# Optimization experiments

Measured on AMD Instinct MI355X. Metric: run time of the kernel, lower is better.

The kernel has to match this reference:

```python
import jax, jax.numpy as jnp
import numpy as np

MESSAGE_PASSES = 3  # constants.message_passes
F_NODE = 64   # hidden_node_features
F_EDGE = 16   # n_edge_features
M_MSG = 64    # message_size
OUT_DIM = 128
B, N = 8, 256
EDGE_DENSITY = 0.1


def setup_inputs() -> dict:
    key = jax.random.key(0)
    ks = jax.random.split(key, 12)
    nodes = jax.random.normal(ks[0], (B, N, F_NODE), dtype=jnp.float32)
    # sparse positive edge features: rand * bernoulli connectivity (avg degree ~ N*density)
    raw = jax.random.uniform(ks[1], (B, N, N, F_EDGE), dtype=jnp.float32)
    conn = (jax.random.uniform(ks[2], (B, N, N)) < EDGE_DENSITY).astype(jnp.float32)
    edges = raw * conn[..., None]
    s = 0.05
    return {
        "nodes": nodes,
        "edges": edges,
        # message MLP: cat(neighbour, edge) -> message_size
        "W_msg": jax.random.normal(ks[3], (F_NODE + F_EDGE, M_MSG), dtype=jnp.float32) * s,
        "b_msg": jnp.zeros((M_MSG,), dtype=jnp.float32),
        # GRU cell (input=message_size, hidden=F_NODE), gates [r|z|n]
        "W_i": jax.random.normal(ks[4], (M_MSG, 3 * F_NODE), dtype=jnp.float32) * s,
        "W_h": jax.random.normal(ks[5], (F_NODE, 3 * F_NODE), dtype=jnp.float32) * s,
        "b_i": jnp.zeros((3 * F_NODE,), dtype=jnp.float32),
        "b_h": jnp.zeros((3 * F_NODE,), dtype=jnp.float32),
        # gated readout
        "W_g": jax.random.normal(ks[6], (2 * F_NODE, OUT_DIM), dtype=jnp.float32) * s,
        "b_g": jnp.zeros((OUT_DIM,), dtype=jnp.float32),
        "W_e": jax.random.normal(ks[7], (F_NODE, OUT_DIM), dtype=jnp.float32) * s,
        "b_e": jnp.zeros((OUT_DIM,), dtype=jnp.float32),
    }


def reference(nodes, edges, W_msg, b_msg, W_i, W_h, b_i, b_h, W_g, b_g, W_e, b_e):
    # adjacency[b,i,j] != 0  <=>  edge (i<-j) exists (original: edges.sum(3).nonzero)
    adjacency = edges.sum(axis=-1)                                   # (B,N,N)
    nbr_mask = (adjacency != 0).astype(nodes.dtype)                  # (B,N,N)
    node_mask = (adjacency.sum(axis=-1) != 0)                        # (B,N) bool
    node_mask_f = node_mask.astype(nodes.dtype)

    h = nodes                                                        # hidden_nodes init = nodes
    b, n, f = nodes.shape
    for _ in range(MESSAGE_PASSES):
        # message_terms over all (node i, neighbour j) pairs; masked sum == padded-gather sum
        nghb = jnp.broadcast_to(h[:, None, :, :], (b, n, n, f))      # (B,N,N,F) neighbour feats
        feat = jnp.concatenate([nghb, edges], axis=-1)               # (B,N,N,F+E)
        terms = jax.nn.relu(feat @ W_msg + b_msg)                    # (B,N,N,M)
        messages = jnp.einsum('bijm,bij->bim', terms, nbr_mask)      # summation aggregation
        # GRU cell update
        gi = messages @ W_i + b_i                                    # (B,N,3F)
        gh = h @ W_h + b_h
        ir, iz, inn = jnp.split(gi, 3, axis=-1)
        hr, hz, hn = jnp.split(gh, 3, axis=-1)
        r = jax.nn.sigmoid(ir + hr)
        z = jax.nn.sigmoid(iz + hz)
        ng = jnp.tanh(inn + r * hn)
        h_new = (1.0 - z) * ng + z * h
        # only nodes with nonzero degree are scattered back (original indexes node_batch idc)
        h = jnp.where(node_mask[..., None], h_new, h)

    # gated readout: sum_i mask_i * sigmoid(g([h_i, x_i])) * e(h_i)
    gate = jax.nn.sigmoid(jnp.concatenate([h, nodes], axis=-1) @ W_g + b_g)  # (B,N,OUT)
    emb = h @ W_e + b_e                                                      # (B,N,OUT)
    out = jnp.einsum('bno,bn->bo', gate * emb, node_mask_f)                  # (B,OUT)
    return out
```

## Files before the change

### kernel.cpp

```cpp
#include <hip/hip_runtime.h>

#define BB 8
#define NN 256
#define FF 64
#define EE 16
#define MM 64
#define G3 192
#define OUTD 128
#define ROWS (BB*NN)
#define MAXD 64

__device__ __forceinline__ float sigmoidf_(float x) {
    return 1.0f / (1.0f + __expf(-x));
}

__global__ __launch_bounds__(512, 4) void k_p0(
    const float* __restrict__ nodes, const float* __restrict__ edges,
    const float* __restrict__ Wmsg, const float* __restrict__ bmsg,
    const float* __restrict__ Wi,   const float* __restrict__ Wh,
    const float* __restrict__ bi,   const float* __restrict__ bh,
    int* __restrict__ deg, int* __restrict__ nbr, float* __restrict__ gef,
    float* __restrict__ h, float* __restrict__ hn_out, float* __restrict__ out)
{
    const int r0  = blockIdx.x * 2;
    const int b   = r0 >> 8;
    const int tid = threadIdx.x;
    const int w   = tid >> 6;
    const int lane = tid & 63;

    __shared__ int   snbr[2][MAXD];
    __shared__ int   sdeg[2];
    __shared__ __align__(16) float efeat[2][MAXD][EE];
    __shared__ float swm[FF][MM];
    __shared__ float part[8][MM];
    __shared__ float smsg[2][MM];
    __shared__ float shold[2][FF];
    __shared__ float gI[2][3][FF], gH[2][3][FF];

    if (blockIdx.x == 0) { out[tid] = 0.0f; out[tid + 512] = 0.0f; }
    if (tid < 2) sdeg[tid] = 0;
    if (tid < 2 * FF) {
        int r = tid >> 6;
        shold[r][tid & 63] = nodes[(size_t)(r0 + r) * FF + (tid & 63)];
    }
    for (int i = tid; i < FF * MM; i += 512) swm[i >> 6][i & 63] = Wmsg[i];
    __syncthreads();

    const float4* base4 = (const float4*)(edges + (size_t)r0 * NN * EE);
    #pragma unroll
    for (int it = 0; it < 4; ++it) {
        int p  = it * 512 + tid;
        float4 v = base4[p];
        int e  = it * 128 + (tid >> 2);
        int rr = e >> 8;
        int j  = e & 255;
        int q  = lane & 3;
        float s4 = v.x + v.y + v.z + v.w;
        s4 += __shfl_xor(s4, 1);
        s4 += __shfl_xor(s4, 2);
        bool pred = (s4 != 0.0f);
        unsigned long long mk = __ballot(pred && (q == 0));
        int cnt = __popcll(mk);
        int base = 0;
        if (lane == 0) base = atomicAdd(&sdeg[rr], cnt);
        base = __shfl(base, 0);
        int slot = base + __popcll(mk & ((1ull << (lane & ~3)) - 1ull));
        if (pred && slot < MAXD) {
            ((float4*)efeat[rr][slot])[q] = v;
            ((float4*)(gef + ((size_t)(r0 + rr) * MAXD + slot) * EE))[q] = v;
            if (q == 0) {
                snbr[rr][slot] = j;
                nbr[(r0 + rr) * MAXD + slot] = j;
            }
        }
    }
    __syncthreads();
    if (tid < 2) {
        int t = sdeg[tid]; t = t < MAXD ? t : MAXD;
        sdeg[tid] = t;
        deg[r0 + tid] = t;
    }
    float we[EE];
    #pragma unroll
    for (int k = 0; k < EE; ++k) we[k] = Wmsg[(FF + k) * MM + lane];
    float bm = bmsg[lane];
    __syncthreads();

    {
        int r = w >> 2, sub = w & 3;
        int d = sdeg[r];
        const float* nball = nodes + (size_t)b * NN * FF;
        float acc = 0.0f;
        for (int s2 = sub; s2 < d; s2 += 8) {
            int sB = s2 + 4;
            bool h2 = (sB < d);
            int jA = snbr[r][s2];
            int jB = h2 ? snbr[r][sB] : jA;
            const float4* na  = (const float4*)(nball + jA * FF);
            const float4* nb4 = (const float4*)(nball + jB * FF);
            float tA = bm, tB = bm;
            #pragma unroll
            for (int k = 0; k < EE; ++k) tA += efeat[r][s2][k] * we[k];
            if (h2) {
                #pragma unroll
                for (int k = 0; k < EE; ++k) tB += efeat[r][sB][k] * we[k];
            }
            #pragma unroll
            for (int kq = 0; kq < 16; ++kq) {
                float4 va = na[kq];
                float4 vb = nb4[kq];
                float w0 = swm[4*kq+0][lane], w1 = swm[4*kq+1][lane];
                float w2 = swm[4*kq+2][lane], w3 = swm[4*kq+3][lane];
                tA += va.x*w0 + va.y*w1 + va.z*w2 + va.w*w3;
                tB += vb.x*w0 + vb.y*w1 + vb.z*w2 + vb.w*w3;
            }
            acc += fmaxf(tA, 0.0f);
            if (h2) acc += fmaxf(tB, 0.0f);
        }
        part[w][lane] = acc;
    }
    __syncthreads();
    if ((w & 3) == 0) {
        int r = w >> 2;
        smsg[r][lane] = part[w][lane] + part[w+1][lane]
                      + part[w+2][lane] + part[w+3][lane];
    }
    __syncthreads();

    if (w < 3) {
        float a0 = bi[w * FF + lane], a1 = a0;
        #pragma unroll 4
        for (int k = 0; k < FF; ++k) {
            float wgt = Wi[k * G3 + w * FF + lane];
            a0 += smsg[0][k] * wgt;
            a1 += smsg[1][k] * wgt;
        }
        gI[0][w][lane] = a0; gI[1][w][lane] = a1;
    } else if (w < 6) {
        int g = w - 3;
        float a0 = bh[g * FF + lane], a1 = a0;
        #pragma unroll 4
        for (int k = 0; k < FF; ++k) {
            float wgt = Wh[k * G3 + g * FF + lane];
            a0 += shold[0][k] * wgt;
            a1 += shold[1][k] * wgt;
        }
        gH[0][g][lane] = a0; gH[1][g][lane] = a1;
    }
    __syncthreads();

    if (tid < 2 * FF) {
        int r = tid >> 6, tt = tid & 63;
        float rg = sigmoidf_(gI[r][0][tt] + gH[r][0][tt]);
        float zg = sigmoidf_(gI[r][1][tt] + gH[r][1][tt]);
        float ng = tanhf(gI[r][2][tt] + rg * gH[r][2][tt]);
        float hold = shold[r][tt];
        float hnew = (1.0f - zg) * ng + zg * hold;
        if (sdeg[r] == 0) hnew = hold;
        shold[r][tt] = hnew;
        h[(size_t)(r0 + r) * FF + tt] = hnew;
    }
    __syncthreads();

    {
        int r = w >> 2, kq = w & 3;
        float p = 0.0f;
        #pragma unroll
        for (int kk = 0; kk < 16; ++kk) {
            int k = kq * 16 + kk;
            p += shold[r][k] * swm[k][lane];
        }
        part[w][lane] = p;
    }
    __syncthreads();
    if (tid < 2 * MM) {
        int r = tid >> 6, tt = tid & 63;
        hn_out[(size_t)(r0 + r) * MM + tt] = bmsg[tt]
            + part[r*4+0][tt] + part[r*4+1][tt] + part[r*4+2][tt] + part[r*4+3][tt];
    }
}

__global__ __launch_bounds__(512, 4) void k_p12(
    const float* __restrict__ Wmsg, const float* __restrict__ bmsg,
    const float* __restrict__ Wi, const float* __restrict__ Wh,
    const float* __restrict__ bi, const float* __restrict__ bh,
    const float* __restrict__ nodes,
    const float* __restrict__ Wg, const float* __restrict__ bg,
    const float* __restrict__ We, const float* __restrict__ be,
    const int* __restrict__ deg, const int* __restrict__ nbr,
    const float* __restrict__ gef,
    const float* __restrict__ hn_in, float* __restrict__ hn_out,
    float* __restrict__ h, float* __restrict__ out, int last)
{
    const int r0  = blockIdx.x * 2;
    const int b   = r0 >> 8;
    const int tid = threadIdx.x;
    const int w   = tid >> 6;
    const int lane = tid & 63;

    __shared__ int   snbr[2][MAXD];
    __shared__ int   sdeg[2];
    __shared__ __align__(16) float efeat[2][MAXD][EE];
    __shared__ float part[8][MM];
    __shared__ float smsg[2][MM];
    __shared__ float shold[2][FF];
    __shared__ float sx[2][FF];
    __shared__ float gI[2][3][FF], gH[2][3][FF];
    __shared__ float shnew[2][FF];
    __shared__ float sg[2][OUTD], se[2][OUTD];

    const int d0 = deg[r0], d1 = deg[r0 + 1];
    if (tid == 0) { sdeg[0] = d0; sdeg[1] = d1; }

    if (tid < 2 * MAXD) {
        int r = tid >> 6;
        snbr[r][tid & 63] = nbr[(r0 + r) * MAXD + (tid & 63)];
    }
    if (tid < 2 * FF) {
        int r = tid >> 6;
        shold[r][tid & 63] = h[(size_t)(r0 + r) * FF + (tid & 63)];
    }
    if (last && tid >= 2 * FF && tid < 4 * FF) {
        int r = (tid >> 6) & 1;
        sx[r][tid & 63] = nodes[(size_t)(r0 + r) * FF + (tid & 63)];
    }
    {
        const float4* g0 = (const float4*)(gef + (size_t)r0 * MAXD * EE);
        const float4* g1 = (const float4*)(gef + (size_t)(r0 + 1) * MAXD * EE);
        for (int i = tid; i < d0 * 4; i += 512) ((float4*)efeat[0])[i] = g0[i];
        for (int i = tid; i < d1 * 4; i += 512) ((float4*)efeat[1])[i] = g1[i];
    }
    float we[EE];
    #pragma unroll
    for (int k = 0; k < EE; ++k) we[k] = Wmsg[(FF + k) * MM + lane];
    __syncthreads();

    {
        int r = w >> 2, sub = w & 3;
        int d = sdeg[r];
        const float* hb = hn_in + (size_t)b * NN * MM;
        float acc = 0.0f;
        for (int s = sub; s < d; s += 4) {
            int j = snbr[r][s];
            float term = hb[j * MM + lane];
            #pragma unroll
            for (int k = 0; k < EE; ++k) term += efeat[r][s][k] * we[k];
            acc += fmaxf(term, 0.0f);
        }
        part[w][lane] = acc;
    }
    __syncthreads();
    if ((w & 3) == 0) {
        int r = w >> 2;
        smsg[r][lane] = part[w][lane] + part[w + 1][lane]
                      + part[w + 2][lane] + part[w + 3][lane];
    }
    __syncthreads();

    if (w < 3) {
        float a0 = bi[w * FF + lane], a1 = a0;
        #pragma unroll 4
        for (int k = 0; k < FF; ++k) {
            float wgt = Wi[k * G3 + w * FF + lane];
            a0 += smsg[0][k] * wgt;
            a1 += smsg[1][k] * wgt;
        }
        gI[0][w][lane] = a0; gI[1][w][lane] = a1;
    } else if (w < 6) {
        int g = w - 3;
        float a0 = bh[g * FF + lane], a1 = a0;
        #pragma unroll 4
        for (int k = 0; k < FF; ++k) {
            float wgt = Wh[k * G3 + g * FF + lane];
            a0 += shold[0][k] * wgt;
            a1 += shold[1][k] * wgt;
        }
        gH[0][g][lane] = a0; gH[1][g][lane] = a1;
    }
    __syncthreads();

    if (tid < 2 * FF) {
        int r = tid >> 6, tt = tid & 63;
        float rr = sigmoidf_(gI[r][0][tt] + gH[r][0][tt]);
        float zz = sigmoidf_(gI[r][1][tt] + gH[r][1][tt]);
        float ng = tanhf(gI[r][2][tt] + rr * gH[r][2][tt]);
        float hold = shold[r][tt];
        float hnew = (1.0f - zz) * ng + zz * hold;
        if (sdeg[r] == 0) hnew = hold;
        shnew[r][tt] = hnew;
        h[(size_t)(r0 + r) * FF + tt] = hnew;
    }
    __syncthreads();

    if (!last) {
        {
            int r = w >> 2, kq = w & 3;
            float p = 0.0f;
            #pragma unroll
            for (int kk = 0; kk < 16; ++kk) {
                int k = kq * 16 + kk;
                p += shnew[r][k] * Wmsg[k * MM + lane];
            }
            part[w][lane] = p;
        }
        __syncthreads();
        if (tid < 2 * MM) {
            int r = tid >> 6, tt = tid & 63;
            hn_out[(size_t)(r0 + r) * MM + tt] = bmsg[tt]
                + part[r*4+0][tt] + part[r*4+1][tt] + part[r*4+2][tt] + part[r*4+3][tt];
        }
    } else {
        int grp = tid >> 7, o = tid & 127;
        int r = grp >> 1, kind = grp & 1;
        if (kind == 0) {
            float g = bg[o];
            #pragma unroll 4
            for (int k = 0; k < FF; ++k) g += shnew[r][k] * Wg[k * OUTD + o];
            #pragma unroll 4
            for (int k = 0; k < FF; ++k) g += sx[r][k] * Wg[(FF + k) * OUTD + o];
            sg[r][o] = g;
        } else {
            float e = be[o];
            #pragma unroll 4
            for (int k = 0; k < FF; ++k) e += shnew[r][k] * We[k * OUTD + o];
            se[r][o] = e;
        }
        __syncthreads();
        if (tid < OUTD) {
            float v0 = (sdeg[0] != 0) ? sigmoidf_(sg[0][tid]) * se[0][tid] : 0.0f;
            float v1 = (sdeg[1] != 0) ? sigmoidf_(sg[1][tid]) * se[1][tid] : 0.0f;
            atomicAdd(&out[b * OUTD + tid], v0 + v1);
        }
    }
}

extern "C" void kernel_launch(void* const* d_in, const int* in_sizes, int n_in,
                              void* d_out, int out_size, void* d_ws, size_t ws_size,
                              hipStream_t stream) {
    const float* nodes = (const float*)d_in[0];
    const float* edges = (const float*)d_in[1];
    const float* Wmsg  = (const float*)d_in[2];
    const float* bmsg  = (const float*)d_in[3];
    const float* Wi    = (const float*)d_in[4];
    const float* Wh    = (const float*)d_in[5];
    const float* bi    = (const float*)d_in[6];
    const float* bh    = (const float*)d_in[7];
    const float* Wg    = (const float*)d_in[8];
    const float* bg    = (const float*)d_in[9];
    const float* We    = (const float*)d_in[10];
    const float* be    = (const float*)d_in[11];
    float* out = (float*)d_out;
    char* ws = (char*)d_ws;

    int*   deg  = (int*)ws;
    int*   nbr  = (int*)(ws + 8192);
    float* gef  = (float*)(ws + 8192 + (size_t)ROWS * MAXD * 4);
    float* h    = gef + (size_t)ROWS * MAXD * EE;
    float* hnA  = h   + (size_t)ROWS * FF;
    float* hnB  = hnA + (size_t)ROWS * MM;

    k_p0<<<ROWS/2, 512, 0, stream>>>(nodes, edges, Wmsg, bmsg, Wi, Wh, bi, bh,
                                     deg, nbr, gef, h, hnA, out);
    k_p12<<<ROWS/2, 512, 0, stream>>>(Wmsg, bmsg, Wi, Wh, bi, bh,
                                      nodes, Wg, bg, We, be, deg, nbr, gef,
                                      hnA, hnB, h, out, 0);
    k_p12<<<ROWS/2, 512, 0, stream>>>(Wmsg, bmsg, Wi, Wh, bi, bh,
                                      nodes, Wg, bg, We, be, deg, nbr, gef,
                                      hnB, hnA, h, out, 1);
}
```

Baseline: 172.5 us.

## Split first message pass out of prep kernel and reuse precomputed node projections

The first kernel now only builds the compacted neighbour lists and edge features, copies the initial nodes into h, and precomputes the node projection through the message weights. All three message passes then run through the shared k_p12 kernel, which works from those projections. This drops the per-neighbour 64-wide matmul on raw node features from pass one. The cost is one extra kernel launch and another read of the workspace.

Result: faster. 145.9 us (-15.4%).

```diff
diff --git a/kernel.cpp b/kernel.cpp
--- a/kernel.cpp
+++ b/kernel.cpp
@@ -14,34 +14,29 @@
     return 1.0f / (1.0f + __expf(-x));
 }
 
-__global__ __launch_bounds__(512, 4) void k_p0(
+__global__ __launch_bounds__(512, 4) void k_prep2(
     const float* __restrict__ nodes, const float* __restrict__ edges,
     const float* __restrict__ Wmsg, const float* __restrict__ bmsg,
-    const float* __restrict__ Wi,   const float* __restrict__ Wh,
-    const float* __restrict__ bi,   const float* __restrict__ bh,
     int* __restrict__ deg, int* __restrict__ nbr, float* __restrict__ gef,
     float* __restrict__ h, float* __restrict__ hn_out, float* __restrict__ out)
 {
     const int r0  = blockIdx.x * 2;
-    const int b   = r0 >> 8;
     const int tid = threadIdx.x;
     const int w   = tid >> 6;
     const int lane = tid & 63;
 
-    __shared__ int   snbr[2][MAXD];
     __shared__ int   sdeg[2];
-    __shared__ __align__(16) float efeat[2][MAXD][EE];
     __shared__ float swm[FF][MM];
     __shared__ float part[8][MM];
-    __shared__ float smsg[2][MM];
     __shared__ float shold[2][FF];
-    __shared__ float gI[2][3][FF], gH[2][3][FF];
 
     if (blockIdx.x == 0) { out[tid] = 0.0f; out[tid + 512] = 0.0f; }
     if (tid < 2) sdeg[tid] = 0;
     if (tid < 2 * FF) {
         int r = tid >> 6;
-        shold[r][tid & 63] = nodes[(size_t)(r0 + r) * FF + (tid & 63)];
+        float v = nodes[(size_t)(r0 + r) * FF + (tid & 63)];
+        shold[r][tid & 63] = v;
+        h[(size_t)(r0 + r) * FF + (tid & 63)] = v;
     }
     for (int i = tid; i < FF * MM; i += 512) swm[i >> 6][i & 63] = Wmsg[i];
     __syncthreads();
@@ -66,101 +61,15 @@
         base = __shfl(base, 0);
         int slot = base + __popcll(mk & ((1ull << (lane & ~3)) - 1ull));
         if (pred && slot < MAXD) {
-            ((float4*)efeat[rr][slot])[q] = v;
             ((float4*)(gef + ((size_t)(r0 + rr) * MAXD + slot) * EE))[q] = v;
-            if (q == 0) {
-                snbr[rr][slot] = j;
-                nbr[(r0 + rr) * MAXD + slot] = j;
-            }
+            if (q == 0) nbr[(r0 + rr) * MAXD + slot] = j;
         }
     }
     __syncthreads();
     if (tid < 2) {
         int t = sdeg[tid]; t = t < MAXD ? t : MAXD;
-        sdeg[tid] = t;
         deg[r0 + tid] = t;
     }
-    float we[EE];
-    #pragma unroll
-    for (int k = 0; k < EE; ++k) we[k] = Wmsg[(FF + k) * MM + lane];
-    float bm = bmsg[lane];
-    __syncthreads();
-
-    {
-        int r = w >> 2, sub = w & 3;
-        int d = sdeg[r];
-        const float* nball = nodes + (size_t)b * NN * FF;
-        float acc = 0.0f;
-        for (int s2 = sub; s2 < d; s2 += 8) {
-            int sB = s2 + 4;
-            bool h2 = (sB < d);
-            int jA = snbr[r][s2];
-            int jB = h2 ? snbr[r][sB] : jA;
-            const float4* na  = (const float4*)(nball + jA * FF);
-            const float4* nb4 = (const float4*)(nball + jB * FF);
-            float tA = bm, tB = bm;
-            #pragma unroll
-            for (int k = 0; k < EE; ++k) tA += efeat[r][s2][k] * we[k];
-            if (h2) {
-                #pragma unroll
-                for (int k = 0; k < EE; ++k) tB += efeat[r][sB][k] * we[k];
-            }
-            #pragma unroll
-            for (int kq = 0; kq < 16; ++kq) {
-                float4 va = na[kq];
-                float4 vb = nb4[kq];
-                float w0 = swm[4*kq+0][lane], w1 = swm[4*kq+1][lane];
-                float w2 = swm[4*kq+2][lane], w3 = swm[4*kq+3][lane];
-                tA += va.x*w0 + va.y*w1 + va.z*w2 + va.w*w3;
-                tB += vb.x*w0 + vb.y*w1 + vb.z*w2 + vb.w*w3;
-            }
-            acc += fmaxf(tA, 0.0f);
-            if (h2) acc += fmaxf(tB, 0.0f);
-        }
-        part[w][lane] = acc;
-    }
-    __syncthreads();
-    if ((w & 3) == 0) {
-        int r = w >> 2;
-        smsg[r][lane] = part[w][lane] + part[w+1][lane]
-                      + part[w+2][lane] + part[w+3][lane];
-    }
-    __syncthreads();
-
-    if (w < 3) {
-        float a0 = bi[w * FF + lane], a1 = a0;
-        #pragma unroll 4
-        for (int k = 0; k < FF; ++k) {
-            float wgt = Wi[k * G3 + w * FF + lane];
-            a0 += smsg[0][k] * wgt;
-            a1 += smsg[1][k] * wgt;
-        }
-        gI[0][w][lane] = a0; gI[1][w][lane] = a1;
-    } else if (w < 6) {
-        int g = w - 3;
-        float a0 = bh[g * FF + lane], a1 = a0;
-        #pragma unroll 4
-        for (int k = 0; k < FF; ++k) {
-            float wgt = Wh[k * G3 + g * FF + lane];
-            a0 += shold[0][k] * wgt;
-            a1 += shold[1][k] * wgt;
-        }
-        gH[0][g][lane] = a0; gH[1][g][lane] = a1;
-    }
-    __syncthreads();
-
-    if (tid < 2 * FF) {
-        int r = tid >> 6, tt = tid & 63;
-        float rg = sigmoidf_(gI[r][0][tt] + gH[r][0][tt]);
-        float zg = sigmoidf_(gI[r][1][tt] + gH[r][1][tt]);
-        float ng = tanhf(gI[r][2][tt] + rg * gH[r][2][tt]);
-        float hold = shold[r][tt];
-        float hnew = (1.0f - zg) * ng + zg * hold;
-        if (sdeg[r] == 0) hnew = hold;
-        shold[r][tt] = hnew;
-        h[(size_t)(r0 + r) * FF + tt] = hnew;
-    }
-    __syncthreads();
 
     {
         int r = w >> 2, kq = w & 3;
@@ -359,12 +268,15 @@
     float* hnA  = h   + (size_t)ROWS * FF;
     float* hnB  = hnA + (size_t)ROWS * MM;
 
-    k_p0<<<ROWS/2, 512, 0, stream>>>(nodes, edges, Wmsg, bmsg, Wi, Wh, bi, bh,
-                                     deg, nbr, gef, h, hnA, out);
+    k_prep2<<<ROWS/2, 512, 0, stream>>>(nodes, edges, Wmsg, bmsg,
+                                        deg, nbr, gef, h, hnA, out);
     k_p12<<<ROWS/2, 512, 0, stream>>>(Wmsg, bmsg, Wi, Wh, bi, bh,
                                       nodes, Wg, bg, We, be, deg, nbr, gef,
                                       hnA, hnB, h, out, 0);
     k_p12<<<ROWS/2, 512, 0, stream>>>(Wmsg, bmsg, Wi, Wh, bi, bh,
                                       nodes, Wg, bg, We, be, deg, nbr, gef,
-                                      hnB, hnA, h, out, 1);
-}
+                                      hnB, hnA, h, out, 0);
+    k_p12<<<ROWS/2, 512, 0, stream>>>(Wmsg, bmsg, Wi, Wh, bi, bh,
+                                      nodes, Wg, bg, We, be, deg, nbr, gef,
+                                      hnA, hnB, h, out, 1);
+}
```
